# Performance work log

Measured on AMD Instinct MI355X. Metric: run time of the kernel, lower is better.

Reference implementation:

```python
import jax, jax.numpy as jnp
import numpy as np

NDIM = 3
RADIUS = 0.2
N_POINT = 1024
N_SAMPLE = 32
D_INPUT = 64
D_HIDDEN = [64, 128, 256]
B, N = 8, 16384


def setup_inputs() -> dict:
    key = jax.random.key(0)
    ks = jax.random.split(key, 8)
    xyz = jax.random.uniform(ks[0], (B, NDIM, N), dtype=jnp.float32)
    points = jax.random.normal(ks[1], (B, D_INPUT, N), dtype=jnp.float32)
    # pointwise conv (kernel 1x1) weights: [out, in] plus bias [out]
    c_in = D_INPUT + NDIM
    inp = {"xyz": xyz, "points": points}
    for i, c_out in enumerate(D_HIDDEN):
        scale = 1.0 / np.sqrt(c_in)
        inp[f"w{i}"] = jax.random.uniform(ks[2 + 2 * i], (c_out, c_in), dtype=jnp.float32, minval=-scale, maxval=scale)
        inp[f"b{i}"] = jax.random.uniform(ks[3 + 2 * i], (c_out,), dtype=jnp.float32, minval=-scale, maxval=scale)
        c_in = c_out
    return inp


def farthest_point_sample(xyz):
    # xyz: [B, N, 3] -> idx [B, n_point]; deterministic, first index seeds (fps_method='first')
    b, n, _ = xyz.shape

    def step(carry, _):
        dist, farthest = carry  # [B, N], [B]
        centroid = jnp.take_along_axis(xyz, farthest[:, None, None], axis=1)  # [B,1,3]
        d = jnp.sum((xyz - centroid) ** 2, axis=-1)  # [B,N]
        dist = jnp.minimum(dist, d)
        return (dist, jnp.argmax(dist, axis=-1)), farthest

    init = (jnp.full((b, n), jnp.inf, xyz.dtype), jnp.zeros((b,), jnp.int32))
    _, idx = jax.lax.scan(step, init, None, length=N_POINT)
    return idx.T.astype(jnp.int32)  # [B, n_point]


def ball_query(new_xyz, xyz):
    # new_xyz: [B,S,3], xyz: [B,N,3] -> idx [B,S,K]
    n = xyz.shape[1]
    sqr = jnp.sum((new_xyz[:, :, None, :] - xyz[:, None, :, :]) ** 2, axis=-1)  # [B,S,N]
    cand = jnp.where(sqr > RADIUS * RADIUS, n, jnp.arange(n, dtype=jnp.int32))
    idx = jnp.sort(cand, axis=-1)[:, :, :N_SAMPLE]
    first = idx[:, :, :1]
    return jnp.where(idx == n, first, idx)


def sample_and_group(xyz, points):
    # xyz: [B,N,3], points: [B,N,D]
    fps_idx = farthest_point_sample(xyz)                      # [B,S]
    new_xyz = jax.vmap(lambda a, i: a[i])(xyz, fps_idx)       # [B,S,3]
    idx = jax.lax.stop_gradient(ball_query(jax.lax.stop_gradient(new_xyz), jax.lax.stop_gradient(xyz)))  # [B,S,K]
    grouped_xyz = jax.vmap(lambda a, i: a[i])(xyz, idx)       # [B,S,K,3]
    grouped_xyz_norm = grouped_xyz - new_xyz[:, :, None, :]
    grouped_points = jax.vmap(lambda a, i: a[i])(points, idx) # [B,S,K,D]
    new_points = jnp.concatenate([grouped_xyz_norm, grouped_points], axis=-1)  # [B,S,K,3+D]
    return new_xyz, new_points


def reference(xyz, points, w0, b0, w1, b1, w2, b2):
    # xyz: [B,3,N], points: [B,D,N]
    xyz_t = jnp.transpose(xyz, (0, 2, 1))      # [B,N,3]
    pts_t = jnp.transpose(points, (0, 2, 1))   # [B,N,D]
    _, new_points = sample_and_group(xyz_t, pts_t)      # [B,S,K,C]
    x = jnp.transpose(new_points, (0, 3, 2, 1))          # [B,C,K,S]
    for w, b in ((w0, b0), (w1, b1), (w2, b2)):
        x = jax.nn.silu(jnp.einsum('oc,bcks->boks', w, x) + b[None, :, None, None])
    return jnp.mean(x, axis=2)                            # [B, d_hidden[-1], S]
```

## Files before the change

kernel.cpp:

```cpp
#include <hip/hip_runtime.h>
#include <math.h>

#define NPTS 16384
#define NCTR 1024
#define BATCH 8
#define NCELL 512

typedef unsigned long long u64;
typedef unsigned int u32;

__device__ __forceinline__ float sq_dist(float x, float y, float z,
                                         float cx, float cy, float cz) {
  float dx = __fsub_rn(x, cx);
  float dy = __fsub_rn(y, cy);
  float dz = __fsub_rn(z, cz);
  return __fadd_rn(__fadd_rn(__fmul_rn(dx, dx), __fmul_rn(dy, dy)), __fmul_rn(dz, dz));
}

__device__ __forceinline__ float silu_f(float x) {
  return x / (1.0f + __expf(-x));
}

__device__ __forceinline__ u64 kmax(u64 a, u64 b) { return a > b ? a : b; }

__device__ __forceinline__ int morton_cell(float x, float y, float z) {
  int mx = min(7, max(0, (int)(x * 8.0f)));
  int my = min(7, max(0, (int)(y * 8.0f)));
  int mz = min(7, max(0, (int)(z * 8.0f)));
  int m = 0;
#pragma unroll
  for (int k = 0; k < 3; ++k) {
    m |= ((mx >> k) & 1) << (3 * k + 2);
    m |= ((my >> k) & 1) << (3 * k + 1);
    m |= ((mz >> k) & 1) << (3 * k + 0);
  }
  return m;
}

__global__ __launch_bounds__(1024) void sort_kernel(
    const float* __restrict__ xyz, float* __restrict__ sxg,
    float* __restrict__ syg, float* __restrict__ szg, int* __restrict__ sog) {
  const int b = blockIdx.x, t = threadIdx.x;
  const float* X = xyz + (size_t)b * 3 * NPTS;
  const float* Y = X + NPTS;
  const float* Z = X + 2 * NPTS;
  __shared__ int cnt[NCELL];
  __shared__ int off[NCELL];
  __shared__ int start[NCELL];
  __shared__ int so_l[NPTS];
  for (int e = t; e < NCELL; e += 1024) cnt[e] = 0;
  __syncthreads();
#pragma unroll
  for (int j = 0; j < 16; ++j) {
    const int n = t + (j << 10);
    atomicAdd(&cnt[morton_cell(X[n], Y[n], Z[n])], 1);
  }
  __syncthreads();
  if (t < NCELL) off[t] = cnt[t];
  __syncthreads();
  for (int d = 1; d < NCELL; d <<= 1) {
    int v = 0;
    if (t < NCELL) { v = off[t]; if (t >= d) v += off[t - d]; }
    __syncthreads();
    if (t < NCELL) off[t] = v;
    __syncthreads();
  }
  if (t < NCELL) { off[t] -= cnt[t]; start[t] = off[t]; }
  __syncthreads();
#pragma unroll
  for (int j = 0; j < 16; ++j) {
    const int n = t + (j << 10);
    const int pos = atomicAdd(&off[morton_cell(X[n], Y[n], Z[n])], 1);
    so_l[pos] = n;
  }
  __syncthreads();
  if (t < NCELL) {
    const int s0 = start[t], k = cnt[t];
    for (int i2 = 1; i2 < k; ++i2) {
      const int key = so_l[s0 + i2];
      int j2 = i2 - 1;
      while (j2 >= 0 && so_l[s0 + j2] > key) {
        so_l[s0 + j2 + 1] = so_l[s0 + j2];
        --j2;
      }
      so_l[s0 + j2 + 1] = key;
    }
  }
  __syncthreads();
  float* sx = sxg + (size_t)b * NPTS;
  float* sy = syg + (size_t)b * NPTS;
  float* sz = szg + (size_t)b * NPTS;
  int* so = sog + (size_t)b * NPTS;
#pragma unroll
  for (int j = 0; j < 16; ++j) {
    const int pos = t + (j << 10);
    const int n = so_l[pos];
    so[pos] = n;
    sx[pos] = X[n];
    sy[pos] = Y[n];
    sz[pos] = Z[n];
  }
}

#define CH_LIST(F) \
  F(0,a0)  F(1,a1)  F(2,a2)  F(3,a3)  F(4,a0)  F(5,a1)  F(6,a2)  F(7,a3)  \
  F(8,a0)  F(9,a1)  F(10,a2) F(11,a3) F(12,a0) F(13,a1) F(14,a2) F(15,a3)

__global__ __launch_bounds__(1024)
void fps_kernel(const float* __restrict__ xyz, const float* __restrict__ sxg,
                const float* __restrict__ syg, const float* __restrict__ szg,
                const int* __restrict__ sog, int* __restrict__ fps_idx) {
  const int b = blockIdx.x;
  const int t = threadIdx.x;
  const int w = t >> 6, lane = t & 63;
  const float* X = xyz + (size_t)b * 3 * NPTS;
  const float* Y = X + NPTS;
  const float* Z = X + 2 * NPTS;
  const float* SX = sxg + (size_t)b * NPTS;
  const float* SY = syg + (size_t)b * NPTS;
  const float* SZ = szg + (size_t)b * NPTS;
  const int* SO = sog + (size_t)b * NPTS;

  __shared__ float sxy[2 * NPTS];
  __shared__ __align__(16) u64 slot[3][2];
  __shared__ float s_zw[3][16];
  __shared__ int fps_lds[NCTR];

#define DECL_CH(c, acc) float z##c, d##c; u32 lo##c;
  CH_LIST(DECL_CH)
#undef DECL_CH

  const int pbase = (w << 10) + lane;

  float bmnx = __builtin_inff(), bmxx = -__builtin_inff();
  float bmny = __builtin_inff(), bmxy = -__builtin_inff();
  float bmnz = __builtin_inff(), bmxz = -__builtin_inff();

#define INIT_CH(c, acc)                                         \
  {                                                             \
    const int p = pbase + (c << 6);                             \
    const float xv = SX[p], yv = SY[p], zv = SZ[p];             \
    sxy[2 * p] = xv; sxy[2 * p + 1] = yv;                       \
    z##c = zv;                                                  \
    const int o = SO[p];                                        \
    lo##c = ((u32)(16383 - o) << 14) | (u32)p;                  \
    d##c = __builtin_inff();                                    \
    float mnx = xv, mxx = xv, mny = yv, mxy = yv;               \
    float mnz = zv, mxz = zv;                                   \
    _Pragma("unroll")                                           \
    for (int off = 32; off >= 1; off >>= 1) {                   \
      mnx = fminf(mnx, __shfl_xor(mnx, off));                   \
      mxx = fmaxf(mxx, __shfl_xor(mxx, off));                   \
      mny = fminf(mny, __shfl_xor(mny, off));                   \
      mxy = fmaxf(mxy, __shfl_xor(mxy, off));                   \
      mnz = fminf(mnz, __shfl_xor(mnz, off));                   \
      mxz = fmaxf(mxz, __shfl_xor(mxz, off));                   \
    }                                                           \
    if (lane == c) {                                            \
      bmnx = mnx; bmxx = mxx; bmny = mny;                       \
      bmxy = mxy; bmnz = mnz; bmxz = mxz;                       \
    }                                                           \
  }
  CH_LIST(INIT_CH)
#undef INIT_CH

#define PIN_CH(c, acc) asm volatile("" : "+v"(z##c));
  CH_LIST(PIN_CH)
#undef PIN_CH

  if (t < 6) slot[t / 2][t & 1] = 0ull;
  if (t == 0) fps_lds[0] = 0;
  __syncthreads();

  float cx = X[0], cy = Y[0], cz = Z[0];
  float gd = __builtin_inff();
  u64 gkey = 0ull;
  float gz = 0.0f;
  int wmaxch = 0;

#define MK(c) ((((u64)__float_as_uint(d##c)) << 32) | (u64)lo##c)
#define KSEL(ka, za, kb, zb, ko, zo)          \
  {                                           \
    const u64 ka_ = (ka), kb_ = (kb);         \
    const bool g_ = ka_ > kb_;                \
    ko = g_ ? ka_ : kb_;                      \
    zo = g_ ? (za) : (zb);                    \
  }

  for (int i = 1; i < NCTR; ++i) {
    const float ux = fmaxf(fmaxf(__fsub_rn(bmnx, cx), __fsub_rn(cx, bmxx)), 0.0f);
    const float uy = fmaxf(fmaxf(__fsub_rn(bmny, cy), __fsub_rn(cy, bmxy)), 0.0f);
    const float uz = fmaxf(fmaxf(__fsub_rn(bmnz, cz), __fsub_rn(cz, bmxz)), 0.0f);
    const float lb = __fadd_rn(__fadd_rn(__fmul_rn(ux, ux), __fmul_rn(uy, uy)),
                               __fmul_rn(uz, uz));
    const u64 mask = __ballot(!(__fmul_rn(lb, 0.9999f) >= gd));
    if (mask != 0ull) {
#define UPD_CH(c, acc)                                                   \
      {                                                                  \
        const float2 xy = *(const float2*)(sxy + 2 * (pbase + (c << 6)));\
        const float dd = sq_dist(xy.x, xy.y, z##c, cx, cy, cz);          \
        d##c = fminf(d##c, dd);                                          \
      }
      CH_LIST(UPD_CH)
#undef UPD_CH
      if ((mask >> wmaxch) & 1ull) {
        u64 m0, m1, m2, m3, m4, m5, m6, m7, q0, q1, q2, q3, h0, h1, kk;
        float n0, n1, n2, n3, n4, n5, n6, n7, r0, r1, r2, r3, e0, e1, bz;
        KSEL(MK(0), z0, MK(1), z1, m0, n0)    KSEL(MK(2), z2, MK(3), z3, m1, n1)
        KSEL(MK(4), z4, MK(5), z5, m2, n2)    KSEL(MK(6), z6, MK(7), z7, m3, n3)
        KSEL(MK(8), z8, MK(9), z9, m4, n4)    KSEL(MK(10), z10, MK(11), z11, m5, n5)
        KSEL(MK(12), z12, MK(13), z13, m6, n6) KSEL(MK(14), z14, MK(15), z15, m7, n7)
        KSEL(m0, n0, m1, n1, q0, r0)  KSEL(m2, n2, m3, n3, q1, r1)
        KSEL(m4, n4, m5, n5, q2, r2)  KSEL(m6, n6, m7, n7, q3, r3)
        KSEL(q0, r0, q1, r1, h0, e0)  KSEL(q2, r2, q3, r3, h1, e1)
        KSEL(h0, e0, h1, e1, kk, bz)
#pragma unroll
        for (int off = 32; off >= 1; off >>= 1) {
          const u64 ok = __shfl_xor(kk, off);
          const float oz = __shfl_xor(bz, off);
          const bool g_ = ok > kk;
          kk = g_ ? ok : kk;
          bz = g_ ? oz : bz;
        }
        gkey = kk;
        gz = bz;
        gd = __uint_as_float((u32)(gkey >> 32));
        wmaxch = (int)(((u32)gkey >> 6) & 15u);
      }
    }
    const int si = i % 3;
    if (lane == 0) {
      s_zw[si][w] = gz;
      atomicMax(&slot[si][w & 1], gkey);
    }
    if (t == 0) {
      const int nsi = si == 2 ? 0 : si + 1;
      slot[nsi][0] = 0ull;
      slot[nsi][1] = 0ull;
    }
    __syncthreads();

    const u64 m = kmax(slot[si][0], slot[si][1]);
    const u32 lowb = (u32)m;
    const int pw = (int)(lowb & 0x3FFFu);
    if (t == 0) fps_lds[i] = 16383 - (int)((lowb >> 14) & 0x3FFFu);

    const int pu = __builtin_amdgcn_readfirstlane(pw);
    const float2 cxy = *(const float2*)(sxy + 2 * pu);
    cx = cxy.x;
    cy = cxy.y;
    cz = s_zw[si][pu >> 10];
  }
#undef MK
#undef KSEL

  __syncthreads();
  for (int e = t; e < NCTR; e += 1024) fps_idx[b * NCTR + e] = fps_lds[e];
}

__global__ __launch_bounds__(256) void ballq_kernel(const float* __restrict__ xyz,
                                                    const int* __restrict__ fps_idx,
                                                    int* __restrict__ ball_idx) {
  const int gw = (blockIdx.x * 256 + threadIdx.x) >> 6;
  const int lane = threadIdx.x & 63;
  const int b = gw >> 10;
  const float* X = xyz + (size_t)b * 3 * NPTS;
  const float* Y = X + NPTS;
  const float* Z = X + 2 * NPTS;
  const int c = fps_idx[gw];
  const float cx = X[c], cy = Y[c], cz = Z[c];
  int* out = ball_idx + (size_t)gw * 32;
  const float R2 = 0.04f;

  int cnt = 0, first = -1;
  for (int base = 0; base < NPTS; base += 64) {
    const int j = base + lane;
    const float d = sq_dist(X[j], Y[j], Z[j], cx, cy, cz);
    const bool inb = !(d > R2);
    const unsigned long long m = __ballot(inb);
    if (first < 0 && m != 0ull) first = base + __ffsll(m) - 1;
    if (inb) {
      const int pos = cnt + __popcll(m & ((1ull << lane) - 1ull));
      if (pos < 32) out[pos] = j;
    }
    cnt += __popcll(m);
    if (cnt >= 32) break;
  }
  for (int k = cnt + lane; k < 32; k += 64) out[k] = first;
}

__global__ __launch_bounds__(256) void transpose_w_kernel(
    const float* __restrict__ w0, const float* __restrict__ w1,
    const float* __restrict__ w2, float* __restrict__ wt0,
    float* __restrict__ wt1, float* __restrict__ wt2) {
  const int t0 = blockIdx.x * 256 + threadIdx.x;
  const int stride = gridDim.x * 256;
  for (int e = t0; e < 64 * 67; e += stride) {
    int o = e / 67, c = e - o * 67;
    wt0[c * 64 + o] = w0[e];
  }
  for (int e = t0; e < 128 * 64; e += stride) {
    int o = e >> 6, c = e & 63;
    wt1[c * 128 + o] = w1[e];
  }
  for (int e = t0; e < 256 * 128; e += stride) {
    int o = e >> 7, c = e & 127;
    wt2[c * 256 + o] = w2[e];
  }
}

__global__ __launch_bounds__(256, 2) void mlp_kernel(
    const float* __restrict__ xyz, const float* __restrict__ points,
    const int* __restrict__ fps_idx, const int* __restrict__ ball_idx,
    const float* __restrict__ wt0, const float* __restrict__ b0,
    const float* __restrict__ wt1, const float* __restrict__ b1,
    const float* __restrict__ wt2, const float* __restrict__ b2,
    float* __restrict__ out) {
  const int s = blockIdx.x, b = blockIdx.y, t = threadIdx.x;

  __shared__ float A1[64 * 36];
  __shared__ float A2[128 * 36];
  __shared__ float S[8704];
  __shared__ float bias_sh[256];
  __shared__ int jidx[32];
  __shared__ float ctr[3];

  const int g = b * NCTR + s;

  if (t < 32) jidx[t] = ball_idx[(size_t)g * 32 + t];
  if (t < 3) ctr[t] = xyz[((size_t)b * 3 + t) * NPTS + fps_idx[g]];
  float* A0 = S;
  float* Wt0 = S + 67 * 36;
  for (int e = t; e < 67 * 64; e += 256) {
    int c = e >> 6, o = e & 63;
    Wt0[c * 68 + o] = wt0[e];
  }
  if (t < 64) bias_sh[t] = b0[t];
  __syncthreads();

  for (int e = t; e < 67 * 32; e += 256) {
    int c = e >> 5, k = e & 31;
    int j = jidx[k];
    float v;
    if (c < 3)
      v = xyz[((size_t)b * 3 + c) * NPTS + j] - ctr[c];
    else
      v = points[((size_t)b * 64 + (c - 3)) * NPTS + j];
    A0[c * 36 + k] = v;
  }
  __syncthreads();

  {
    const int o0 = (t & 31) * 2;
    const int k0 = (t >> 5) * 4;
    float acc[4][2] = {{0.f, 0.f}, {0.f, 0.f}, {0.f, 0.f}, {0.f, 0.f}};
    for (int c = 0; c < 67; ++c) {
      const float4 a = *(const float4*)(A0 + c * 36 + k0);
      const float wv0 = Wt0[c * 68 + o0];
      const float wv1 = Wt0[c * 68 + o0 + 1];
      acc[0][0] = fmaf(a.x, wv0, acc[0][0]);
      acc[1][0] = fmaf(a.y, wv0, acc[1][0]);
      acc[2][0] = fmaf(a.z, wv0, acc[2][0]);
      acc[3][0] = fmaf(a.w, wv0, acc[3][0]);
      acc[0][1] = fmaf(a.x, wv1, acc[0][1]);
      acc[1][1] = fmaf(a.y, wv1, acc[1][1]);
      acc[2][1] = fmaf(a.z, wv1, acc[2][1]);
      acc[3][1] = fmaf(a.w, wv1, acc[3][1]);
    }
#pragma unroll
    for (int i = 0; i < 2; ++i) {
      const float bb = bias_sh[o0 + i];
      float4 r;
      r.x = silu_f(acc[0][i] + bb);
      r.y = silu_f(acc[1][i] + bb);
      r.z = silu_f(acc[2][i] + bb);
      r.w = silu_f(acc[3][i] + bb);
      *(float4*)(A1 + (o0 + i) * 36 + k0) = r;
    }
  }
  __syncthreads();

  float* Wt1 = S;
  for (int e = t; e < 128 * 64; e += 256) {
    int c = e >> 7, o = e & 127;
    Wt1[c * 132 + o] = wt1[e];
  }
  if (t < 128) bias_sh[t] = b1[t];
  __syncthreads();

  {
    const int o0 = (t & 31) * 4;
    const int k0 = (t >> 5) * 4;
    float acc[4][4];
#pragma unroll
    for (int kk = 0; kk < 4; ++kk)
#pragma unroll
      for (int oo = 0; oo < 4; ++oo) acc[kk][oo] = 0.f;
    for (int c = 0; c < 64; ++c) {
      const float4 a = *(const float4*)(A1 + c * 36 + k0);
      const float4 w = *(const float4*)(Wt1 + c * 132 + o0);
      const float av[4] = {a.x, a.y, a.z, a.w};
      const float wv[4] = {w.x, w.y, w.z, w.w};
#pragma unroll
      for (int kk = 0; kk < 4; ++kk)
#pragma unroll
        for (int oo = 0; oo < 4; ++oo)
          acc[kk][oo] = fmaf(av[kk], wv[oo], acc[kk][oo]);
    }
#pragma unroll
    for (int oo = 0; oo < 4; ++oo) {
      const float bb = bias_sh[o0 + oo];
      float4 r;
      r.x = silu_f(acc[0][oo] + bb);
      r.y = silu_f(acc[1][oo] + bb);
      r.z = silu_f(acc[2][oo] + bb);
      r.w = silu_f(acc[3][oo] + bb);
      *(float4*)(A2 + (o0 + oo) * 36 + k0) = r;
    }
  }
  __syncthreads();

  float* Wt2 = S;
  float* P = A1;
  const int o0 = (t & 31) * 2;
  const int k0 = (t >> 5) * 4;
  const int kg = t >> 5;
  for (int chunk = 0; chunk < 4; ++chunk) {
    for (int e = t; e < 64 * 128; e += 256) {
      int c = e >> 6, o = e & 63;
      Wt2[c * 68 + o] = wt2[c * 256 + chunk * 64 + o];
    }
    if (t < 64) bias_sh[t] = b2[chunk * 64 + t];
    __syncthreads();

    float acc[4][2] = {{0.f, 0.f}, {0.f, 0.f}, {0.f, 0.f}, {0.f, 0.f}};
    for (int c = 0; c < 128; ++c) {
      const float4 a = *(const float4*)(A2 + c * 36 + k0);
      const float wv0 = Wt2[c * 68 + o0];
      const float wv1 = Wt2[c * 68 + o0 + 1];
      acc[0][0] = fmaf(a.x, wv0, acc[0][0]);
      acc[1][0] = fmaf(a.y, wv0, acc[1][0]);
      acc[2][0] = fmaf(a.z, wv0, acc[2][0]);
      acc[3][0] = fmaf(a.w, wv0, acc[3][0]);
      acc[0][1] = fmaf(a.x, wv1, acc[0][1]);
      acc[1][1] = fmaf(a.y, wv1, acc[1][1]);
      acc[2][1] = fmaf(a.z, wv1, acc[2][1]);
      acc[3][1] = fmaf(a.w, wv1, acc[3][1]);
    }
#pragma unroll
    for (int i = 0; i < 2; ++i) {
      const float bb = bias_sh[o0 + i];
      float sum = silu_f(acc[0][i] + bb) + silu_f(acc[1][i] + bb) +
                  silu_f(acc[2][i] + bb) + silu_f(acc[3][i] + bb);
      P[(o0 + i) * 9 + kg] = sum;
    }
    __syncthreads();
    if (t < 64) {
      float tot = 0.f;
#pragma unroll
      for (int q = 0; q < 8; ++q) tot += P[t * 9 + q];
      out[((size_t)b * 256 + chunk * 64 + t) * NCTR + s] = tot * (1.0f / 32.0f);
    }
    __syncthreads();
  }
}

extern "C" void kernel_launch(void* const* d_in, const int* in_sizes, int n_in,
                              void* d_out, int out_size, void* d_ws, size_t ws_size,
                              hipStream_t stream) {
  const float* xyz = (const float*)d_in[0];
  const float* points = (const float*)d_in[1];
  const float* w0 = (const float*)d_in[2];
  const float* b0 = (const float*)d_in[3];
  const float* w1 = (const float*)d_in[4];
  const float* b1 = (const float*)d_in[5];
  const float* w2 = (const float*)d_in[6];
  const float* b2 = (const float*)d_in[7];
  float* out = (float*)d_out;

  int* fps = (int*)d_ws;
  int* bidx = (int*)d_ws + 8192;
  float* wt0 = (float*)d_ws + 270336;
  float* wt1 = wt0 + 67 * 64;
  float* wt2 = wt1 + 64 * 128;
  float* sxg = (float*)d_ws + 315584;
  float* syg = sxg + BATCH * NPTS;
  float* szg = syg + BATCH * NPTS;
  int* sog = (int*)(szg + BATCH * NPTS);

  transpose_w_kernel<<<64, 256, 0, stream>>>(w0, w1, w2, wt0, wt1, wt2);
  sort_kernel<<<BATCH, 1024, 0, stream>>>(xyz, sxg, syg, szg, sog);
  fps_kernel<<<BATCH, 1024, 0, stream>>>(xyz, sxg, syg, szg, sog, fps);
  ballq_kernel<<<2048, 256, 0, stream>>>(xyz, fps, bidx);
  mlp_kernel<<<dim3(NCTR, BATCH), 256, 0, stream>>>(xyz, points, fps, bidx,
                                                    wt0, b0, wt1, b1, wt2, b2, out);
}
```

Baseline: 1.959 ms.

## Interleave FPS point chunks across waves and skip pruned chunks per-mask

Changes how spatially sorted points map to waves and chunks: chunk c of wave w now holds points c*1024 + w*64 + lane, so each lane-ballot bit corresponds to one chunk. When few chunks can improve (popcount < 6), the distance update runs only for the chunks whose bounding-box test passed, instead of updating all 16 chunks. This skips LDS reads and math for pruned chunks. The cost is extra branching and a changed wave-level locality of points, which may weaken the bounding-box pruning.

```diff
diff --git a/kernel.cpp b/kernel.cpp
--- a/kernel.cpp
+++ b/kernel.cpp
@@ -130,7 +130,7 @@
   CH_LIST(DECL_CH)
 #undef DECL_CH
 
-  const int pbase = (w << 10) + lane;
+  const int wbase = (w << 6) + lane;
 
   float bmnx = __builtin_inff(), bmxx = -__builtin_inff();
   float bmny = __builtin_inff(), bmxy = -__builtin_inff();
@@ -138,7 +138,7 @@
 
 #define INIT_CH(c, acc)                                         \
   {                                                             \
-    const int p = pbase + (c << 6);                             \
+    const int p = ((c) << 10) + wbase;                          \
     const float xv = SX[p], yv = SY[p], zv = SZ[p];             \
     sxy[2 * p] = xv; sxy[2 * p + 1] = yv;                       \
     z##c = zv;                                                  \
@@ -193,17 +193,31 @@
     const float uz = fmaxf(fmaxf(__fsub_rn(bmnz, cz), __fsub_rn(cz, bmxz)), 0.0f);
     const float lb = __fadd_rn(__fadd_rn(__fmul_rn(ux, ux), __fmul_rn(uy, uy)),
                                __fmul_rn(uz, uz));
-    const u64 mask = __ballot(!(__fmul_rn(lb, 0.9999f) >= gd));
-    if (mask != 0ull) {
-#define UPD_CH(c, acc)                                                   \
-      {                                                                  \
-        const float2 xy = *(const float2*)(sxy + 2 * (pbase + (c << 6)));\
-        const float dd = sq_dist(xy.x, xy.y, z##c, cx, cy, cz);          \
-        d##c = fminf(d##c, dd);                                          \
+    const u32 mask = (u32)__ballot(!(__fmul_rn(lb, 0.9999f) >= gd));
+    if (mask != 0u) {
+      if (__builtin_popcount(mask) >= 6) {
+#define UPDU_CH(c, acc)                                                  \
+        {                                                                \
+          const float2 xy =                                              \
+              *(const float2*)(sxy + 2 * (((c) << 10) + wbase));         \
+          const float dd = sq_dist(xy.x, xy.y, z##c, cx, cy, cz);        \
+          d##c = fminf(d##c, dd);                                        \
+        }
+        CH_LIST(UPDU_CH)
+#undef UPDU_CH
+      } else {
+#define UPDG_CH(c, acc)                                                  \
+        if (mask & (1u << (c))) {                                        \
+          const float2 xy =                                              \
+              *(const float2*)(sxy + 2 * (((c) << 10) + wbase));         \
+          float dd = sq_dist(xy.x, xy.y, z##c, cx, cy, cz);              \
+          asm volatile("" : "+v"(dd));                                   \
+          d##c = fminf(d##c, dd);                                        \
+        }
+        CH_LIST(UPDG_CH)
+#undef UPDG_CH
       }
-      CH_LIST(UPD_CH)
-#undef UPD_CH
-      if ((mask >> wmaxch) & 1ull) {
+      if ((mask >> wmaxch) & 1u) {
         u64 m0, m1, m2, m3, m4, m5, m6, m7, q0, q1, q2, q3, h0, h1, kk;
         float n0, n1, n2, n3, n4, n5, n6, n7, r0, r1, r2, r3, e0, e1, bz;
         KSEL(MK(0), z0, MK(1), z1, m0, n0)    KSEL(MK(2), z2, MK(3), z3, m1, n1)
@@ -225,7 +239,7 @@
         gkey = kk;
         gz = bz;
         gd = __uint_as_float((u32)(gkey >> 32));
-        wmaxch = (int)(((u32)gkey >> 6) & 15u);
+        wmaxch = (int)(((u32)gkey >> 10) & 15u);
       }
     }
     const int si = i % 3;
@@ -249,7 +263,7 @@
     const float2 cxy = *(const float2*)(sxy + 2 * pu);
     cx = cxy.x;
     cy = cxy.y;
-    cz = s_zw[si][pu >> 10];
+    cz = s_zw[si][(pu >> 6) & 15];
   }
 #undef MK
 #undef KSEL
```

New measurement: 1.892 ms. 3.5% less time.
